# Optimization experiments

Hardware: AMD Instinct MI355X
Metric: run time of the kernel (lower is better)

## Reference

```python
import jax, jax.numpy as jnp
import numpy as np

B, H, LQ, LKV, D = 2, 4, 512, 512, 64


def setup_inputs() -> dict:
    key = jax.random.key(0)
    ks = jax.random.split(key, 6)
    queries = jax.random.normal(ks[0], (B, H, LQ, D), dtype=jnp.float32)
    keys = jax.random.normal(ks[1], (B, H, LKV, D), dtype=jnp.float32)
    values = jax.random.normal(ks[2], (B, H, LKV, D), dtype=jnp.float32)
    mask = jax.random.randint(ks[3], (B, LQ, LKV), 0, 2) > 0  # bool [B, Lq, Lkv]
    # linear_concat: weight [D, 2D] (normal std=0.02), bias zeros
    W_concat = jax.random.normal(ks[4], (D, 2 * D), dtype=jnp.float32) * 0.02
    b_concat = jnp.zeros((D,), dtype=jnp.float32)
    # linear_logit: weight [1, D] -> vector [D], bias scalar zero
    w_logit = jax.random.normal(ks[5], (D,), dtype=jnp.float32) * 0.02
    b_logit = jnp.zeros((), dtype=jnp.float32)
    return dict(queries=queries, keys=keys, values=values, mask=mask,
                W_concat=W_concat, b_concat=b_concat,
                w_logit=w_logit, b_logit=b_logit)


def reference(queries, keys, values, mask, W_concat, b_concat, w_logit, b_logit):
    d = queries.shape[-1]
    # cat(q, k) @ W.T == q @ W[:, :d].T + k @ W[:, d:].T  (exact split of the concat-linear)
    qp = jnp.einsum('bhqd,ed->bhqe', queries, W_concat[:, :d])   # [B,H,Lq,D]
    kp = jnp.einsum('bhkd,ed->bhke', keys, W_concat[:, d:])      # [B,H,Lkv,D]
    combined = jnp.tanh(qp[:, :, :, None, :] + kp[:, :, None, :, :] + b_concat)  # [B,H,Lq,Lkv,D]
    logits = jnp.einsum('bhqke,e->bhqk', combined, w_logit) + b_logit            # [B,H,Lq,Lkv]
    # mask handling: invert; rows fully masked get un-masked (avoid all -inf softmax)
    inv = ~mask  # [B,Lq,Lkv]
    inv = jnp.where(jnp.all(inv, axis=-1, keepdims=True), False, inv)
    inv = inv[:, None, :, :]  # broadcast over heads
    logits = jnp.where(inv, -jnp.inf, logits)
    weights = jax.nn.softmax(logits, axis=-1)
    if weights.shape[1] == 1:  # torch .squeeze(dim=1) semantics
        weights = jnp.squeeze(weights, axis=1)
    return weights
```

## Files before the change

kernel.cpp:

```cpp
#include <hip/hip_runtime.h>
#include <hip/hip_bf16.h>


#define NQROWS 4096

__global__ __launch_bounds__(256) void proj_kernel(
    const float* __restrict__ Q, const float* __restrict__ K,
    const float* __restrict__ W, const float* __restrict__ bC,
    float* __restrict__ eq, float* __restrict__ ekt)
{
  const int t  = threadIdx.x;
  const int tr = t >> 6;
  const int e  = t & 63;
  const int rbase = blockIdx.x * 16;
  const bool isK = rbase >= NQROWS;
  const int r0 = isK ? rbase - NQROWS : rbase;
  const float* __restrict__ src = isK ? K : Q;
  const int off = isK ? 64 : 0;

  __shared__ float  srow[16][64];
  __shared__ float4 wsh[64][16];

  for (int i = t; i < 16 * 64; i += 256)
    srow[i >> 6][i & 63] = src[(r0 + (i >> 6)) * 64 + (i & 63)];
  for (int i = t; i < 64 * 16; i += 256) {
    const int er = i >> 4, d4 = i & 15;
    wsh[er][d4 ^ (er & 7)] =
        reinterpret_cast<const float4*>(W + er * 128 + off)[d4];
  }
  __syncthreads();

  float acc0 = 0.f, acc1 = 0.f, acc2 = 0.f, acc3 = 0.f;
  const int rA = tr * 4;
  #pragma unroll
  for (int d4 = 0; d4 < 16; ++d4) {
    const float4 w4 = wsh[e][d4 ^ (e & 7)];
    const float4 s0 = *reinterpret_cast<const float4*>(&srow[rA + 0][d4 * 4]);
    const float4 s1 = *reinterpret_cast<const float4*>(&srow[rA + 1][d4 * 4]);
    const float4 s2 = *reinterpret_cast<const float4*>(&srow[rA + 2][d4 * 4]);
    const float4 s3 = *reinterpret_cast<const float4*>(&srow[rA + 3][d4 * 4]);
    acc0 = fmaf(s0.x, w4.x, acc0); acc0 = fmaf(s0.y, w4.y, acc0);
    acc0 = fmaf(s0.z, w4.z, acc0); acc0 = fmaf(s0.w, w4.w, acc0);
    acc1 = fmaf(s1.x, w4.x, acc1); acc1 = fmaf(s1.y, w4.y, acc1);
    acc1 = fmaf(s1.z, w4.z, acc1); acc1 = fmaf(s1.w, w4.w, acc1);
    acc2 = fmaf(s2.x, w4.x, acc2); acc2 = fmaf(s2.y, w4.y, acc2);
    acc2 = fmaf(s2.z, w4.z, acc2); acc2 = fmaf(s2.w, w4.w, acc2);
    acc3 = fmaf(s3.x, w4.x, acc3); acc3 = fmaf(s3.y, w4.y, acc3);
    acc3 = fmaf(s3.z, w4.z, acc3); acc3 = fmaf(s3.w, w4.w, acc3);
  }

  const float C2 = 2.8853900817779268f;
  if (!isK) {
    const float bias = bC[e];
    eq[(r0 + rA + 0) * 64 + e] = __builtin_amdgcn_exp2f((acc0 + bias) * C2);
    eq[(r0 + rA + 1) * 64 + e] = __builtin_amdgcn_exp2f((acc1 + bias) * C2);
    eq[(r0 + rA + 2) * 64 + e] = __builtin_amdgcn_exp2f((acc2 + bias) * C2);
    eq[(r0 + rA + 3) * 64 + e] = __builtin_amdgcn_exp2f((acc3 + bias) * C2);
  } else {
    const int bh = (r0 + rA) >> 9;
    const int k0 = (r0 + rA) & 511;
    float* __restrict__ dst = ekt + bh * 64 * 512 + e * 512 + k0;
    dst[0] = __builtin_amdgcn_exp2f(acc0 * C2);
    dst[1] = __builtin_amdgcn_exp2f(acc1 * C2);
    dst[2] = __builtin_amdgcn_exp2f(acc2 * C2);
    dst[3] = __builtin_amdgcn_exp2f(acc3 * C2);
  }
}

__global__ __launch_bounds__(256) void attn_kernel(
    const float* __restrict__ eq, const float* __restrict__ ekt,
    const float* __restrict__ wl, const int* __restrict__ mask,
    float* __restrict__ out)
{
  const int t  = threadIdx.x;
  const int w  = t >> 6;
  const int tk = t & 63;
  const int bh = blockIdx.x >> 7;
  const int qb = blockIdx.x & 127;
  const int b  = bh >> 2;
  const int q  = qb * 4 + w;

  __shared__ float qsh[4][64];
  __shared__ float w2s[64];
  if (t < 64) w2s[t] = -2.0f * wl[t];
  qsh[w][tk] = eq[(bh * 512 + q) * 64 + tk];
  __syncthreads();

  const float4* __restrict__ kb4 =
      reinterpret_cast<const float4*>(ekt + bh * 64 * 512);

  float4 a0 = {0.f, 0.f, 0.f, 0.f};
  float4 a1 = {0.f, 0.f, 0.f, 0.f};

#define EVAL1(QE, WE, E)                                                      \
  {                                                                           \
    const float4 k0 = kb4[(E) * 128 + tk];                                    \
    const float4 k1 = kb4[(E) * 128 + 64 + tk];                               \
    a0.x = fmaf((WE), __builtin_amdgcn_rcpf(fmaf((QE), k0.x, 1.f)), a0.x);    \
    a0.y = fmaf((WE), __builtin_amdgcn_rcpf(fmaf((QE), k0.y, 1.f)), a0.y);    \
    a0.z = fmaf((WE), __builtin_amdgcn_rcpf(fmaf((QE), k0.z, 1.f)), a0.z);    \
    a0.w = fmaf((WE), __builtin_amdgcn_rcpf(fmaf((QE), k0.w, 1.f)), a0.w);    \
    a1.x = fmaf((WE), __builtin_amdgcn_rcpf(fmaf((QE), k1.x, 1.f)), a1.x);    \
    a1.y = fmaf((WE), __builtin_amdgcn_rcpf(fmaf((QE), k1.y, 1.f)), a1.y);    \
    a1.z = fmaf((WE), __builtin_amdgcn_rcpf(fmaf((QE), k1.z, 1.f)), a1.z);    \
    a1.w = fmaf((WE), __builtin_amdgcn_rcpf(fmaf((QE), k1.w, 1.f)), a1.w);    \
  }

  #pragma unroll 2
  for (int e4 = 0; e4 < 16; ++e4) {
    const float4 q4 = *reinterpret_cast<const float4*>(&qsh[w][e4 * 4]);
    const float4 w4 = *reinterpret_cast<const float4*>(&w2s[e4 * 4]);
    EVAL1(q4.x, w4.x, e4 * 4 + 0)
    EVAL1(q4.y, w4.y, e4 * 4 + 1)
    EVAL1(q4.z, w4.z, e4 * 4 + 2)
    EVAL1(q4.w, w4.w, e4 * 4 + 3)
  }

  const int* __restrict__ mrow = mask + (b * 512 + q) * 512;
  const int4 m0 = *reinterpret_cast<const int4*>(mrow + 4 * tk);
  const int4 m1 = *reinterpret_cast<const int4*>(mrow + 256 + 4 * tk);
  const int lo = m0.x | m0.y | m0.z | m0.w | m1.x | m1.y | m1.z | m1.w;
  const bool rowany = __any(lo != 0);
  const float NEG = -__builtin_inff();
  if (rowany) {
    if (m0.x == 0) a0.x = NEG;
    if (m0.y == 0) a0.y = NEG;
    if (m0.z == 0) a0.z = NEG;
    if (m0.w == 0) a0.w = NEG;
    if (m1.x == 0) a1.x = NEG;
    if (m1.y == 0) a1.y = NEG;
    if (m1.z == 0) a1.z = NEG;
    if (m1.w == 0) a1.w = NEG;
  }

  float mm = fmaxf(fmaxf(fmaxf(a0.x, a0.y), fmaxf(a0.z, a0.w)),
                   fmaxf(fmaxf(a1.x, a1.y), fmaxf(a1.z, a1.w)));
  #pragma unroll
  for (int s = 1; s < 64; s <<= 1) mm = fmaxf(mm, __shfl_xor(mm, s));

  const float L2E = 1.4426950408889634f;
  const float c = mm * L2E;
  float p[8];
  p[0] = __builtin_amdgcn_exp2f(fmaf(a0.x, L2E, -c));
  p[1] = __builtin_amdgcn_exp2f(fmaf(a0.y, L2E, -c));
  p[2] = __builtin_amdgcn_exp2f(fmaf(a0.z, L2E, -c));
  p[3] = __builtin_amdgcn_exp2f(fmaf(a0.w, L2E, -c));
  p[4] = __builtin_amdgcn_exp2f(fmaf(a1.x, L2E, -c));
  p[5] = __builtin_amdgcn_exp2f(fmaf(a1.y, L2E, -c));
  p[6] = __builtin_amdgcn_exp2f(fmaf(a1.z, L2E, -c));
  p[7] = __builtin_amdgcn_exp2f(fmaf(a1.w, L2E, -c));
  float sum = 0.f;
  #pragma unroll
  for (int j = 0; j < 8; ++j) sum += p[j];
  #pragma unroll
  for (int s = 1; s < 64; s <<= 1) sum += __shfl_xor(sum, s);
  const float inv = 1.0f / sum;

  float* __restrict__ o = out + (bh * 512 + q) * 512;
  float4 o0 = {p[0] * inv, p[1] * inv, p[2] * inv, p[3] * inv};
  float4 o1 = {p[4] * inv, p[5] * inv, p[6] * inv, p[7] * inv};
  *reinterpret_cast<float4*>(o + 4 * tk) = o0;
  *reinterpret_cast<float4*>(o + 256 + 4 * tk) = o1;
}

extern "C" void kernel_launch(void* const* d_in, const int* in_sizes, int n_in,
                              void* d_out, int out_size, void* d_ws, size_t ws_size,
                              hipStream_t stream) {
  const float* Q  = (const float*)d_in[0];
  const float* K  = (const float*)d_in[1];
  const int*   M  = (const int*)d_in[3];
  const float* W  = (const float*)d_in[4];
  const float* bC = (const float*)d_in[5];
  const float* wl = (const float*)d_in[6];
  float* out = (float*)d_out;
  float* eqbuf  = (float*)d_ws;
  float* ektbuf = eqbuf + NQROWS * 64;

  proj_kernel<<<512, 256, 0, stream>>>(Q, K, W, bC, eqbuf, ektbuf);
  attn_kernel<<<1024, 256, 0, stream>>>(eqbuf, ektbuf, wl, M, out);
}
```

Before: 31.14 us.

## Combine four tanh terms per reciprocal and split each query row across two waves

Result: no change. 30.65 us (-1.6%).

```diff
diff --git a/kernel.cpp b/kernel.cpp
--- a/kernel.cpp
+++ b/kernel.cpp
@@ -67,7 +67,7 @@
   }
 }
 
-__global__ __launch_bounds__(256) void attn_kernel(
+__global__ __launch_bounds__(512) void attn_kernel(
     const float* __restrict__ eq, const float* __restrict__ ekt,
     const float* __restrict__ wl, const int* __restrict__ mask,
     float* __restrict__ out)
@@ -75,92 +75,96 @@
   const int t  = threadIdx.x;
   const int w  = t >> 6;
   const int tk = t & 63;
+  const int rw = w >> 1;
+  const int h  = w & 1;
   const int bh = blockIdx.x >> 7;
   const int qb = blockIdx.x & 127;
   const int b  = bh >> 2;
-  const int q  = qb * 4 + w;
+  const int q  = qb * 4 + rw;
 
   __shared__ float qsh[4][64];
   __shared__ float w2s[64];
+  __shared__ float s_any[8], s_mmax[8], s_rmax[8], s_sum[8];
+
   if (t < 64) w2s[t] = -2.0f * wl[t];
-  qsh[w][tk] = eq[(bh * 512 + q) * 64 + tk];
+  if (h == 0) qsh[rw][tk] = eq[(bh * 512 + q) * 64 + tk];
   __syncthreads();
 
-  const float4* __restrict__ kb4 =
-      reinterpret_cast<const float4*>(ekt + bh * 64 * 512);
+  const float4* __restrict__ kq =
+      reinterpret_cast<const float4*>(ekt + bh * 64 * 512) + h * 64 + tk;
 
-  float4 a0 = {0.f, 0.f, 0.f, 0.f};
-  float4 a1 = {0.f, 0.f, 0.f, 0.f};
+  float4 acc = {0.f, 0.f, 0.f, 0.f};
 
-#define EVAL1(QE, WE, E)                                                      \
+#define QUADC(C)                                                              \
   {                                                                           \
-    const float4 k0 = kb4[(E) * 128 + tk];                                    \
-    const float4 k1 = kb4[(E) * 128 + 64 + tk];                               \
-    a0.x = fmaf((WE), __builtin_amdgcn_rcpf(fmaf((QE), k0.x, 1.f)), a0.x);    \
-    a0.y = fmaf((WE), __builtin_amdgcn_rcpf(fmaf((QE), k0.y, 1.f)), a0.y);    \
-    a0.z = fmaf((WE), __builtin_amdgcn_rcpf(fmaf((QE), k0.z, 1.f)), a0.z);    \
-    a0.w = fmaf((WE), __builtin_amdgcn_rcpf(fmaf((QE), k0.w, 1.f)), a0.w);    \
-    a1.x = fmaf((WE), __builtin_amdgcn_rcpf(fmaf((QE), k1.x, 1.f)), a1.x);    \
-    a1.y = fmaf((WE), __builtin_amdgcn_rcpf(fmaf((QE), k1.y, 1.f)), a1.y);    \
-    a1.z = fmaf((WE), __builtin_amdgcn_rcpf(fmaf((QE), k1.z, 1.f)), a1.z);    \
-    a1.w = fmaf((WE), __builtin_amdgcn_rcpf(fmaf((QE), k1.w, 1.f)), a1.w);    \
+    const float t0 = fmaf(q4.x, K0.C, 1.f);                                   \
+    const float t1 = fmaf(q4.y, K1.C, 1.f);                                   \
+    const float t2 = fmaf(q4.z, K2.C, 1.f);                                   \
+    const float t3 = fmaf(q4.w, K3.C, 1.f);                                   \
+    const float t01 = t0 * t1, t23 = t2 * t3;                                 \
+    const float den = t01 * t23;                                              \
+    const float n01 = fmaf(w4.x, t1, w4.y * t0);                              \
+    const float n23 = fmaf(w4.z, t3, w4.w * t2);                              \
+    const float num = fmaf(n01, t23, n23 * t01);                              \
+    acc.C = fmaf(num, __builtin_amdgcn_rcpf(den), acc.C);                     \
   }
 
   #pragma unroll 2
-  for (int e4 = 0; e4 < 16; ++e4) {
-    const float4 q4 = *reinterpret_cast<const float4*>(&qsh[w][e4 * 4]);
-    const float4 w4 = *reinterpret_cast<const float4*>(&w2s[e4 * 4]);
-    EVAL1(q4.x, w4.x, e4 * 4 + 0)
-    EVAL1(q4.y, w4.y, e4 * 4 + 1)
-    EVAL1(q4.z, w4.z, e4 * 4 + 2)
-    EVAL1(q4.w, w4.w, e4 * 4 + 3)
+  for (int eb = 0; eb < 16; ++eb) {
+    const float4 q4 = *reinterpret_cast<const float4*>(&qsh[rw][eb * 4]);
+    const float4 w4 = *reinterpret_cast<const float4*>(&w2s[eb * 4]);
+    const float4 K0 = kq[(eb * 4 + 0) * 128];
+    const float4 K1 = kq[(eb * 4 + 1) * 128];
+    const float4 K2 = kq[(eb * 4 + 2) * 128];
+    const float4 K3 = kq[(eb * 4 + 3) * 128];
+    QUADC(x) QUADC(y) QUADC(z) QUADC(w)
   }
 
-  const int* __restrict__ mrow = mask + (b * 512 + q) * 512;
-  const int4 m0 = *reinterpret_cast<const int4*>(mrow + 4 * tk);
-  const int4 m1 = *reinterpret_cast<const int4*>(mrow + 256 + 4 * tk);
-  const int lo = m0.x | m0.y | m0.z | m0.w | m1.x | m1.y | m1.z | m1.w;
-  const bool rowany = __any(lo != 0);
+  const int* __restrict__ mrow = mask + (b * 512 + q) * 512 + h * 256;
+  const int4 mv = *reinterpret_cast<const int4*>(mrow + 4 * tk);
+  const int lo = mv.x | mv.y | mv.z | mv.w;
+  const float hany = __any(lo != 0) ? 1.0f : 0.0f;
+
   const float NEG = -__builtin_inff();
-  if (rowany) {
-    if (m0.x == 0) a0.x = NEG;
-    if (m0.y == 0) a0.y = NEG;
-    if (m0.z == 0) a0.z = NEG;
-    if (m0.w == 0) a0.w = NEG;
-    if (m1.x == 0) a1.x = NEG;
-    if (m1.y == 0) a1.y = NEG;
-    if (m1.z == 0) a1.z = NEG;
-    if (m1.w == 0) a1.w = NEG;
+  float4 am = acc;
+  if (mv.x == 0) am.x = NEG;
+  if (mv.y == 0) am.y = NEG;
+  if (mv.z == 0) am.z = NEG;
+  if (mv.w == 0) am.w = NEG;
+
+  float rmax = fmaxf(fmaxf(acc.x, acc.y), fmaxf(acc.z, acc.w));
+  float mmax = fmaxf(fmaxf(am.x, am.y), fmaxf(am.z, am.w));
+  #pragma unroll
+  for (int s = 1; s < 64; s <<= 1) {
+    rmax = fmaxf(rmax, __shfl_xor(rmax, s));
+    mmax = fmaxf(mmax, __shfl_xor(mmax, s));
   }
+  if (tk == 0) { s_any[w] = hany; s_mmax[w] = mmax; s_rmax[w] = rmax; }
+  __syncthreads();
 
-  float mm = fmaxf(fmaxf(fmaxf(a0.x, a0.y), fmaxf(a0.z, a0.w)),
-                   fmaxf(fmaxf(a1.x, a1.y), fmaxf(a1.z, a1.w)));
-  #pragma unroll
-  for (int s = 1; s < 64; s <<= 1) mm = fmaxf(mm, __shfl_xor(mm, s));
+  const int wp = w & ~1;
+  const bool rowany = (s_any[wp] + s_any[wp + 1]) > 0.0f;
+  const float m = rowany ? fmaxf(s_mmax[wp], s_mmax[wp + 1])
+                         : fmaxf(s_rmax[wp], s_rmax[wp + 1]);
+  const float4 av = rowany ? am : acc;
 
   const float L2E = 1.4426950408889634f;
-  const float c = mm * L2E;
-  float p[8];
-  p[0] = __builtin_amdgcn_exp2f(fmaf(a0.x, L2E, -c));
-  p[1] = __builtin_amdgcn_exp2f(fmaf(a0.y, L2E, -c));
-  p[2] = __builtin_amdgcn_exp2f(fmaf(a0.z, L2E, -c));
-  p[3] = __builtin_amdgcn_exp2f(fmaf(a0.w, L2E, -c));
-  p[4] = __builtin_amdgcn_exp2f(fmaf(a1.x, L2E, -c));
-  p[5] = __builtin_amdgcn_exp2f(fmaf(a1.y, L2E, -c));
-  p[6] = __builtin_amdgcn_exp2f(fmaf(a1.z, L2E, -c));
-  p[7] = __builtin_amdgcn_exp2f(fmaf(a1.w, L2E, -c));
-  float sum = 0.f;
-  #pragma unroll
-  for (int j = 0; j < 8; ++j) sum += p[j];
+  const float c = m * L2E;
+  float4 p;
+  p.x = __builtin_amdgcn_exp2f(fmaf(av.x, L2E, -c));
+  p.y = __builtin_amdgcn_exp2f(fmaf(av.y, L2E, -c));
+  p.z = __builtin_amdgcn_exp2f(fmaf(av.z, L2E, -c));
+  p.w = __builtin_amdgcn_exp2f(fmaf(av.w, L2E, -c));
+  float sum = p.x + p.y + p.z + p.w;
   #pragma unroll
   for (int s = 1; s < 64; s <<= 1) sum += __shfl_xor(sum, s);
-  const float inv = 1.0f / sum;
+  if (tk == 0) s_sum[w] = sum;
+  __syncthreads();
 
-  float* __restrict__ o = out + (bh * 512 + q) * 512;
-  float4 o0 = {p[0] * inv, p[1] * inv, p[2] * inv, p[3] * inv};
-  float4 o1 = {p[4] * inv, p[5] * inv, p[6] * inv, p[7] * inv};
-  *reinterpret_cast<float4*>(o + 4 * tk) = o0;
-  *reinterpret_cast<float4*>(o + 256 + 4 * tk) = o1;
+  const float inv = 1.0f / (s_sum[wp] + s_sum[wp + 1]);
+  float4 o4 = {p.x * inv, p.y * inv, p.z * inv, p.w * inv};
+  float* __restrict__ o = out + (bh * 512 + q) * 512 + h * 256;
+  *reinterpret_cast<float4*>(o + 4 * tk) = o4;
 }
 
 extern "C" void kernel_launch(void* const* d_in, const int* in_sizes, int n_in,
@@ -177,5 +181,5 @@
   float* ektbuf = eqbuf + NQROWS * 64;
 
   proj_kernel<<<512, 256, 0, stream>>>(Q, K, W, bC, eqbuf, ektbuf);
-  attn_kernel<<<1024, 256, 0, stream>>>(eqbuf, ektbuf, wl, M, out);
+  attn_kernel<<<1024, 512, 0, stream>>>(eqbuf, ektbuf, wl, M, out);
 }
```
